# Kernel tuning notes

Measured on AMD Instinct MI355X. Metric: run time of the kernel, lower is better.

The kernel has to match this reference:

```python
import jax, jax.numpy as jnp
import numpy as np

KH = KW = 3
STRIDE = 1
PAD = 1
DIL = 1


def _bilinear_sample(img, py, px):
    Hin, Win = img.shape[-2], img.shape[-1]
    y0 = jnp.floor(py)
    x0 = jnp.floor(px)
    y0i = y0.astype(jnp.int32)
    x0i = x0.astype(jnp.int32)
    wy = py - y0
    wx = px - x0

    def get(yi, xi):
        valid = (yi >= 0) & (yi < Hin) & (xi >= 0) & (xi < Win)
        yc = jnp.clip(yi, 0, Hin - 1)
        xc = jnp.clip(xi, 0, Win - 1)
        v = img[:, yc, xc]  # [C, K, H, W]
        return v * valid[None].astype(img.dtype)

    v00 = get(y0i, x0i)
    v01 = get(y0i, x0i + 1)
    v10 = get(y0i + 1, x0i)
    v11 = get(y0i + 1, x0i + 1)
    return (v00 * (1 - wy) * (1 - wx) + v01 * (1 - wy) * wx
            + v10 * wy * (1 - wx) + v11 * wy * wx)  # [C, K, H, W]


def _deform_conv(input, offset, mask, weight, bias):
    B, C, H, W = input.shape
    outH = (H + 2 * PAD - DIL * (KH - 1) - 1) // STRIDE + 1
    outW = (W + 2 * PAD - DIL * (KW - 1) - 1) // STRIDE + 1
    K = KH * KW
    # NOTE: DepthOffset in the original source overwrites its computed
    # depth-guided offsets with zeros and detaches them, so the effective
    # sampling offset is just `offset` (standard modulated deform conv, DCNv2).
    off = offset.reshape(B, K, 2, outH, outW)
    off_y = off[:, :, 0]  # [B, K, outH, outW]
    off_x = off[:, :, 1]
    ky = (jnp.arange(K) // KW) * DIL  # kernel-tap row offsets
    kx = (jnp.arange(K) % KW) * DIL
    ys = jnp.arange(outH) * STRIDE - PAD
    xs = jnp.arange(outW) * STRIDE - PAD
    base_y = (ky[:, None, None] + ys[None, :, None]).astype(input.dtype)  # [K, outH, 1]
    base_x = (kx[:, None, None] + xs[None, None, :]).astype(input.dtype)  # [K, 1, outW]
    py = base_y[None] + off_y  # [B, K, outH, outW]
    px = base_x[None] + off_x
    cols = jax.vmap(_bilinear_sample)(input, py, px)  # [B, C, K, outH, outW]
    cols = cols * mask[:, None]  # modulate by mask [B, 1, K, outH, outW]
    out = jnp.einsum('bckhw,ock->bohw', cols, weight.reshape(weight.shape[0], C, K))
    return out + bias[None, :, None, None]


def setup_inputs() -> dict:
    key = jax.random.key(0)
    ks = jax.random.split(key, 6)
    B, C, H, W = 4, 64, 128, 128
    O = 64
    fan_in = C * KH * KW
    bound = 1.0 / np.sqrt(fan_in)
    return {
        'input': jax.random.normal(ks[0], (B, C, H, W), dtype=jnp.float32),
        'depth': jax.random.uniform(ks[1], (B, 1, H, W), dtype=jnp.float32),
        'offset': jax.random.normal(ks[2], (B, 18, H, W), dtype=jnp.float32),
        'mask': jax.random.uniform(ks[3], (B, 9, H, W), dtype=jnp.float32),
        'weight': jax.random.uniform(ks[4], (O, C, KH, KW), dtype=jnp.float32,
                                     minval=-bound, maxval=bound),
        'bias': jax.random.uniform(ks[5], (O,), dtype=jnp.float32,
                                   minval=-bound, maxval=bound),
    }


def reference(input, depth, offset, mask, weight, bias):
    # depth-guided offsets are computed then zeroed+detached in the original
    # module, so depth does not influence the output.
    return _deform_conv(input, offset, mask, weight, bias)
```

## Files before the change

### kernel.cpp

```cpp
#include <hip/hip_runtime.h>


typedef __attribute__((ext_vector_type(8))) short bf16x8;
typedef __attribute__((ext_vector_type(4))) float f32x4;
typedef __attribute__((ext_vector_type(4))) unsigned int u32x4;

#define HH 128
#define WW 128
#define CC 64
#define OO 64
#define HW (128 * 128)

__device__ __forceinline__ unsigned f32_to_bf16_rne(float f) {
    unsigned u = __float_as_uint(f);
    return (u + 0x7FFFu + ((u >> 16) & 1u)) >> 16;
}

__global__ __launch_bounds__(256)
void prep_fused11(const float* __restrict__ input,
                  unsigned short* __restrict__ nhwc,
                  const float* __restrict__ weight,
                  unsigned short* __restrict__ wT2)
{
    __shared__ unsigned tile[64][33];
    const int tid = threadIdx.x;
    const int blk = blockIdx.x;

    if (blk >= 2048) {
        const int d  = (blk - 2048) * 256 + tid;
        const int o  = d & 63;
        const int k8 = d >> 6;
        const int kt = k8 >> 3;
        const int c8 = k8 & 7;
        u32x4 pk;
        #pragma unroll
        for (int jj = 0; jj < 4; ++jj) {
            unsigned lo = f32_to_bf16_rne(weight[o * 576 + (c8 * 8 + 2 * jj)     * 9 + kt]);
            unsigned hi = f32_to_bf16_rne(weight[o * 576 + (c8 * 8 + 2 * jj + 1) * 9 + kt]);
            pk[jj] = lo | (hi << 16);
        }
        *(u32x4*)(wT2 + (size_t)d * 8) = pk;
        return;
    }

    const int b  = blk >> 9;
    const int y  = (blk >> 2) & 127;
    const int xbase = (blk & 3) * 32;
    #pragma unroll
    for (int it = 0; it < 8; ++it) {
        int flat = it * 256 + tid;
        int c = flat >> 5, x = flat & 31;
        float v = input[((b * 64 + c) * 128 + y) * 128 + xbase + x];
        tile[c][x] = f32_to_bf16_rne(v);
    }
    __syncthreads();
    {
        int x = tid >> 3, cg = tid & 7;
        unsigned r0 = tile[cg * 8 + 0][x], r1 = tile[cg * 8 + 1][x];
        unsigned r2 = tile[cg * 8 + 2][x], r3 = tile[cg * 8 + 3][x];
        unsigned r4 = tile[cg * 8 + 4][x], r5 = tile[cg * 8 + 5][x];
        unsigned r6 = tile[cg * 8 + 6][x], r7 = tile[cg * 8 + 7][x];
        u32x4 pk;
        pk[0] = r0 | (r1 << 16); pk[1] = r2 | (r3 << 16);
        pk[2] = r4 | (r5 << 16); pk[3] = r6 | (r7 << 16);
        *(u32x4*)(nhwc + ((size_t)((b * 128 + y) * 128 + xbase + x)) * 64 + cg * 8) = pk;
    }
}

__global__ __launch_bounds__(512, 2)
void ddc_win11(const unsigned short* __restrict__ nhwc,
               const unsigned short* __restrict__ wT2,
               const float* __restrict__ offset,
               const float* __restrict__ mask,
               const float* __restrict__ bias,
               float* __restrict__ out)
{
    __shared__ u32x4 win[8192];

    const int blk0 = blockIdx.x;
    const int blk  = (blk0 & 7) * 64 + (blk0 >> 3);
    const int b    = blk >> 7;
    const int h    = blk & 127;
    const int tid  = threadIdx.x;
    const int wave = tid >> 6;
    const int lane = tid & 63;
    const int l15  = lane & 15;
    const int kq   = lane >> 4;
    const int wpix = wave * 16 + l15;

    f32x4 acc[4];
    #pragma unroll
    for (int mt = 0; mt < 4; ++mt) acc[mt] = (f32x4){0.f, 0.f, 0.f, 0.f};

    const unsigned short* nb = nhwc + (size_t)b * HW * CC;
    const u32x4* wsrc = (const u32x4*)wT2;

    float oyv[9], oxv[9], mv[9];
    #pragma unroll
    for (int kt = 0; kt < 9; ++kt) {
        oyv[kt] = offset[((b * 18 + 2 * kt)     * 128 + h) * 128 + wpix];
        oxv[kt] = offset[((b * 18 + 2 * kt + 1) * 128 + h) * 128 + wpix];
        mv[kt]  = mask  [((b * 9  + kt)         * 128 + h) * 128 + wpix];
    }

    #pragma unroll
    for (int i = 0; i < 16; ++i) {
        const int slot = i >> 1;
        const int y = h - 3 + slot;
        if (y >= 0 && y < HH) {
            const int q  = ((i & 1) << 9) + tid;
            const int x  = q >> 3;
            const int c8 = q & 7;
            win[slot * 1024 + q] =
                *(const u32x4*)(nb + ((size_t)(y * WW + x)) * CC + ((c8 ^ (x & 7)) << 3));
        }
    }
    __syncthreads();

    auto do_tap = [&](int kt, float oy, float ox, float m) {
        const float py = (float)(h - 1 + kt / 3) + oy;
        const float px = (float)(wpix - 1 + kt % 3) + ox;
        const float y0f = floorf(py), x0f = floorf(px);
        const int y0 = (int)y0f, x0 = (int)x0f;
        const float wy = py - y0f, wx = px - x0f;
        const int y1 = y0 + 1, x1 = x0 + 1;
        const bool vy0 = (y0 >= 0) & (y0 < HH);
        const bool vy1 = (y1 >= 0) & (y1 < HH);
        const bool vx0 = (x0 >= 0) & (x0 < WW);
        const bool vx1 = (x1 >= 0) & (x1 < WW);
        const int y0c = min(max(y0, 0), HH - 1), y1c = min(max(y1, 0), HH - 1);
        const int x0c = min(max(x0, 0), WW - 1), x1c = min(max(x1, 0), WW - 1);
        const float wy1 = 1.f - wy, wx1 = 1.f - wx;
        const float c00 = (vy0 && vx0) ? wy1 * wx1 * m : 0.f;
        const float c01 = (vy0 && vx1) ? wy1 * wx  * m : 0.f;
        const float c10 = (vy1 && vx0) ? wy  * wx1 * m : 0.f;
        const float c11 = (vy1 && vx1) ? wy  * wx  * m : 0.f;

        const int s0 = y0c - (h - 3), s1 = y1c - (h - 3);
        const bool in0 = ((unsigned)s0 < 8u);
        const bool in1 = ((unsigned)s1 < 8u);
        const int r0 = (in0 ? s0 : 0) * 1024;
        const int r1 = (in1 ? s1 : 0) * 1024;
        const int bx0 = x0c * 8, sx0 = x0c & 7;
        const int bx1 = x1c * 8, sx1 = x1c & 7;

        #pragma unroll
        for (int ks = 0; ks < 2; ++ks) {
            const int ch = ks * 4 + kq;

            u32x4 w00 = win[r0 + bx0 + (ch ^ sx0)];
            u32x4 w01 = win[r0 + bx1 + (ch ^ sx1)];
            u32x4 w10 = win[r1 + bx0 + (ch ^ sx0)];
            u32x4 w11 = win[r1 + bx1 + (ch ^ sx1)];
            if (!in0) {
                w00 = *(const u32x4*)(nb + ((size_t)y0c * WW + x0c) * CC + ch * 8);
                w01 = *(const u32x4*)(nb + ((size_t)y0c * WW + x1c) * CC + ch * 8);
            }
            if (!in1) {
                w10 = *(const u32x4*)(nb + ((size_t)y1c * WW + x0c) * CC + ch * 8);
                w11 = *(const u32x4*)(nb + ((size_t)y1c * WW + x1c) * CC + ch * 8);
            }

            u32x4 pk;
            #pragma unroll
            for (int j = 0; j < 4; ++j) {
                const float a0 = __uint_as_float(w00[j] << 16);
                const float a1 = __uint_as_float(w00[j] & 0xFFFF0000u);
                const float b0 = __uint_as_float(w01[j] << 16);
                const float b1 = __uint_as_float(w01[j] & 0xFFFF0000u);
                const float d0 = __uint_as_float(w10[j] << 16);
                const float d1 = __uint_as_float(w10[j] & 0xFFFF0000u);
                const float e0 = __uint_as_float(w11[j] << 16);
                const float e1 = __uint_as_float(w11[j] & 0xFFFF0000u);
                const float s0f = c00 * a0 + c01 * b0 + c10 * d0 + c11 * e0;
                const float s1f = c00 * a1 + c01 * b1 + c10 * d1 + c11 * e1;
                pk[j] = f32_to_bf16_rne(s0f) | (f32_to_bf16_rne(s1f) << 16);
            }
            const bf16x8 bfrag = __builtin_bit_cast(bf16x8, pk);

            #pragma unroll
            for (int mt = 0; mt < 4; ++mt) {
                const bf16x8 afrag = __builtin_bit_cast(bf16x8,
                    wsrc[(kt * 8 + ks * 4 + kq) * 64 + mt * 16 + l15]);
                acc[mt] = __builtin_amdgcn_mfma_f32_16x16x32_bf16(afrag, bfrag, acc[mt], 0, 0, 0);
            }
        }
    };

    #pragma unroll
    for (int kt = 0; kt < 9; ++kt) {
        do_tap(kt, oyv[kt], oxv[kt], mv[kt]);
    }

    #pragma unroll
    for (int mt = 0; mt < 4; ++mt) {
        const f32x4 bv = *(const f32x4*)(bias + mt * 16 + kq * 4);
        #pragma unroll
        for (int r = 0; r < 4; ++r) {
            const int o = mt * 16 + kq * 4 + r;
            out[((b * 64 + o) * 128 + h) * 128 + wpix] = acc[mt][r] + bv[r];
        }
    }
}

extern "C" void kernel_launch(void* const* d_in, const int* in_sizes, int n_in,
                              void* d_out, int out_size, void* d_ws, size_t ws_size,
                              hipStream_t stream)
{
    const float* input  = (const float*)d_in[0];
    const float* offset = (const float*)d_in[2];
    const float* mask   = (const float*)d_in[3];
    const float* weight = (const float*)d_in[4];
    const float* bias   = (const float*)d_in[5];
    float* out = (float*)d_out;

    unsigned short* nhwc = (unsigned short*)d_ws;
    unsigned short* wT2  = nhwc + (size_t)4 * HW * CC;

    prep_fused11<<<dim3(2066), dim3(256), 0, stream>>>(input, nhwc, weight, wT2);
    ddc_win11<<<dim3(512), dim3(512), 0, stream>>>(nhwc, wT2, offset, mask, bias, out);
}
```

Before: 109.6 us.

## Roll tap loop and stage offset/mask rows in shared memory

Offset and mask values for the output row are loaded cooperatively into shared memory instead of 27 per-thread registers. The 9-tap loop is no longer unrolled, and each iteration loads its weight fragments and all corner samples up front. The aim is lower register pressure and code size, plus earlier issue of loads within each tap. In exchange, it loses cross-tap instruction scheduling and adds LDS traffic for the stencil values.

```diff
diff --git a/kernel.cpp b/kernel.cpp
--- a/kernel.cpp
+++ b/kernel.cpp
@@ -17,7 +17,7 @@
 }
 
 __global__ __launch_bounds__(256)
-void prep_fused11(const float* __restrict__ input,
+void prep_fused14(const float* __restrict__ input,
                   unsigned short* __restrict__ nhwc,
                   const float* __restrict__ weight,
                   unsigned short* __restrict__ wT2)
@@ -68,14 +68,15 @@
 }
 
 __global__ __launch_bounds__(512, 2)
-void ddc_win11(const unsigned short* __restrict__ nhwc,
-               const unsigned short* __restrict__ wT2,
-               const float* __restrict__ offset,
-               const float* __restrict__ mask,
-               const float* __restrict__ bias,
-               float* __restrict__ out)
+void ddc_roll14(const unsigned short* __restrict__ nhwc,
+                const unsigned short* __restrict__ wT2,
+                const float* __restrict__ offset,
+                const float* __restrict__ mask,
+                const float* __restrict__ bias,
+                float* __restrict__ out)
 {
     __shared__ u32x4 win[8192];
+    __shared__ float sten[3456];
 
     const int blk0 = blockIdx.x;
     const int blk  = (blk0 & 7) * 64 + (blk0 >> 3);
@@ -95,12 +96,17 @@
     const unsigned short* nb = nhwc + (size_t)b * HW * CC;
     const u32x4* wsrc = (const u32x4*)wT2;
 
-    float oyv[9], oxv[9], mv[9];
-    #pragma unroll
-    for (int kt = 0; kt < 9; ++kt) {
-        oyv[kt] = offset[((b * 18 + 2 * kt)     * 128 + h) * 128 + wpix];
-        oxv[kt] = offset[((b * 18 + 2 * kt + 1) * 128 + h) * 128 + wpix];
-        mv[kt]  = mask  [((b * 9  + kt)         * 128 + h) * 128 + wpix];
+    #pragma unroll
+    for (int it = 0; it < 7; ++it) {
+        const int f = it * 512 + tid;
+        if (f < 2304) {
+            const int j = f >> 7, x = f & 127;
+            sten[f] = offset[((b * 18 + j) * 128 + h) * 128 + x];
+        } else if (f < 3456) {
+            const int g = f - 2304;
+            const int j = g >> 7, x = g & 127;
+            sten[f] = mask[((b * 9 + j) * 128 + h) * 128 + x];
+        }
     }
 
     #pragma unroll
@@ -117,9 +123,20 @@
     }
     __syncthreads();
 
-    auto do_tap = [&](int kt, float oy, float ox, float m) {
-        const float py = (float)(h - 1 + kt / 3) + oy;
-        const float px = (float)(wpix - 1 + kt % 3) + ox;
+    int ky = 0, kx = 0;
+    #pragma unroll 1
+    for (int kt = 0; kt < 9; ++kt) {
+        const u32x4* wp0 = wsrc + (kt * 8 + kq) * 64 + l15;
+        const u32x4* wp1 = wsrc + (kt * 8 + 4 + kq) * 64 + l15;
+        const u32x4 wa0 = wp0[0],  wa1 = wp0[16], wa2 = wp0[32], wa3 = wp0[48];
+        const u32x4 wb0 = wp1[0],  wb1 = wp1[16], wb2 = wp1[32], wb3 = wp1[48];
+
+        const float oy = sten[((2 * kt)     << 7) + wpix];
+        const float ox = sten[((2 * kt + 1) << 7) + wpix];
+        const float m  = sten[2304 + (kt << 7) + wpix];
+
+        const float py = (float)(h - 1 + ky) + oy;
+        const float px = (float)(wpix - 1 + kx) + ox;
         const float y0f = floorf(py), x0f = floorf(px);
         const int y0 = (int)y0f, x0 = (int)x0f;
         const float wy = py - y0f, wx = px - x0f;
@@ -144,23 +161,35 @@
         const int bx0 = x0c * 8, sx0 = x0c & 7;
         const int bx1 = x1c * 8, sx1 = x1c & 7;
 
+        const int ch0 = kq, ch1 = 4 + kq;
+        u32x4 a00 = win[r0 + bx0 + (ch0 ^ sx0)];
+        u32x4 a01 = win[r0 + bx1 + (ch0 ^ sx1)];
+        u32x4 a10 = win[r1 + bx0 + (ch0 ^ sx0)];
+        u32x4 a11 = win[r1 + bx1 + (ch0 ^ sx1)];
+        u32x4 b00 = win[r0 + bx0 + (ch1 ^ sx0)];
+        u32x4 b01 = win[r0 + bx1 + (ch1 ^ sx1)];
+        u32x4 b10 = win[r1 + bx0 + (ch1 ^ sx0)];
+        u32x4 b11 = win[r1 + bx1 + (ch1 ^ sx1)];
+
+        if (!in0) {
+            a00 = *(const u32x4*)(nb + ((size_t)y0c * WW + x0c) * CC + ch0 * 8);
+            a01 = *(const u32x4*)(nb + ((size_t)y0c * WW + x1c) * CC + ch0 * 8);
+            b00 = *(const u32x4*)(nb + ((size_t)y0c * WW + x0c) * CC + ch1 * 8);
+            b01 = *(const u32x4*)(nb + ((size_t)y0c * WW + x1c) * CC + ch1 * 8);
+        }
+        if (!in1) {
+            a10 = *(const u32x4*)(nb + ((size_t)y1c * WW + x0c) * CC + ch0 * 8);
+            a11 = *(const u32x4*)(nb + ((size_t)y1c * WW + x1c) * CC + ch0 * 8);
+            b10 = *(const u32x4*)(nb + ((size_t)y1c * WW + x0c) * CC + ch1 * 8);
+            b11 = *(const u32x4*)(nb + ((size_t)y1c * WW + x1c) * CC + ch1 * 8);
+        }
+
         #pragma unroll
         for (int ks = 0; ks < 2; ++ks) {
-            const int ch = ks * 4 + kq;
-
-            u32x4 w00 = win[r0 + bx0 + (ch ^ sx0)];
-            u32x4 w01 = win[r0 + bx1 + (ch ^ sx1)];
-            u32x4 w10 = win[r1 + bx0 + (ch ^ sx0)];
-            u32x4 w11 = win[r1 + bx1 + (ch ^ sx1)];
-            if (!in0) {
-                w00 = *(const u32x4*)(nb + ((size_t)y0c * WW + x0c) * CC + ch * 8);
-                w01 = *(const u32x4*)(nb + ((size_t)y0c * WW + x1c) * CC + ch * 8);
-            }
-            if (!in1) {
-                w10 = *(const u32x4*)(nb + ((size_t)y1c * WW + x0c) * CC + ch * 8);
-                w11 = *(const u32x4*)(nb + ((size_t)y1c * WW + x1c) * CC + ch * 8);
-            }
-
+            const u32x4 w00 = ks ? b00 : a00;
+            const u32x4 w01 = ks ? b01 : a01;
+            const u32x4 w10 = ks ? b10 : a10;
+            const u32x4 w11 = ks ? b11 : a11;
             u32x4 pk;
             #pragma unroll
             for (int j = 0; j < 4; ++j) {
@@ -177,19 +206,17 @@
                 pk[j] = f32_to_bf16_rne(s0f) | (f32_to_bf16_rne(s1f) << 16);
             }
             const bf16x8 bfrag = __builtin_bit_cast(bf16x8, pk);
-
-            #pragma unroll
-            for (int mt = 0; mt < 4; ++mt) {
-                const bf16x8 afrag = __builtin_bit_cast(bf16x8,
-                    wsrc[(kt * 8 + ks * 4 + kq) * 64 + mt * 16 + l15]);
-                acc[mt] = __builtin_amdgcn_mfma_f32_16x16x32_bf16(afrag, bfrag, acc[mt], 0, 0, 0);
-            }
-        }
-    };
-
-    #pragma unroll
-    for (int kt = 0; kt < 9; ++kt) {
-        do_tap(kt, oyv[kt], oxv[kt], mv[kt]);
+            const bf16x8 af0 = __builtin_bit_cast(bf16x8, ks ? wb0 : wa0);
+            const bf16x8 af1 = __builtin_bit_cast(bf16x8, ks ? wb1 : wa1);
+            const bf16x8 af2 = __builtin_bit_cast(bf16x8, ks ? wb2 : wa2);
+            const bf16x8 af3 = __builtin_bit_cast(bf16x8, ks ? wb3 : wa3);
+            acc[0] = __builtin_amdgcn_mfma_f32_16x16x32_bf16(af0, bfrag, acc[0], 0, 0, 0);
+            acc[1] = __builtin_amdgcn_mfma_f32_16x16x32_bf16(af1, bfrag, acc[1], 0, 0, 0);
+            acc[2] = __builtin_amdgcn_mfma_f32_16x16x32_bf16(af2, bfrag, acc[2], 0, 0, 0);
+            acc[3] = __builtin_amdgcn_mfma_f32_16x16x32_bf16(af3, bfrag, acc[3], 0, 0, 0);
+        }
+
+        if (++kx == 3) { kx = 0; ++ky; }
     }
 
     #pragma unroll
@@ -217,6 +244,6 @@
     unsigned short* nhwc = (unsigned short*)d_ws;
     unsigned short* wT2  = nhwc + (size_t)4 * HW * CC;
 
-    prep_fused11<<<dim3(2066), dim3(256), 0, stream>>>(input, nhwc, weight, wT2);
-    ddc_win11<<<dim3(512), dim3(512), 0, stream>>>(nhwc, wT2, offset, mask, bias, out);
-}
+    prep_fused14<<<dim3(2066), dim3(256), 0, stream>>>(input, nhwc, weight, wT2);
+    ddc_roll14<<<dim3(512), dim3(512), 0, stream>>>(nhwc, wT2, offset, mask, bias, out);
+}
```

Result: no change. 110.3 us (+0.7%).
